# Kernel optimization log

Measured on AMD Instinct MI355X. Metric: run time of the kernel, lower is better.

Reference implementation:

```python
import jax, jax.numpy as jnp
import numpy as np

N_ROOMS = 300
N = N_ROOMS + 2          # state dim: 2 envelope nodes + rooms
M = N_ROOMS + 1          # input dim: [Tout; Q per room]
T = 60000                # number of t_eval points
DT = 30.0                # seconds between solution points
N_KNOTS = 2001           # Tout interpolation knots
ONE_THIRD = 1.0 / 3.0


def setup_inputs() -> dict:
    key = jax.random.key(0)
    k1, k2, k3, k4 = jax.random.split(key, 4)
    n_params = N * N + N_ROOMS
    params = jax.random.uniform(k1, (n_params,), jnp.float32)
    theta_lo = jnp.zeros((n_params,), jnp.float32)
    # conductance-like entries kept tiny so RK4 with h=30s stays stable
    theta_hi = jnp.concatenate([
        jnp.full((N * N,), 1e-4, jnp.float32),
        jnp.ones((N_ROOMS,), jnp.float32),
    ])
    B = jax.random.normal(k2, (N, M), jnp.float32) * 1e-3  # constant input matrix
    tout_t = jnp.linspace(0.0, T * DT, N_KNOTS).astype(jnp.float32)
    tout_vals = 15.0 + 10.0 * jax.random.normal(k3, (N_KNOTS,), jnp.float32)
    iv = 15.0 + 10.0 * jax.random.uniform(k4, (N, 1), jnp.float32)
    t_eval = jnp.arange(T, dtype=jnp.float32) * DT
    return {"params": params, "theta_lo": theta_lo, "theta_hi": theta_hi,
            "B": B, "tout_t": tout_t, "tout_vals": tout_vals,
            "iv": iv, "t_eval": t_eval, "t0": 0}


def reference(params, theta_lo, theta_hi, B, tout_t, tout_vals, iv, t_eval, t0):
    # transform + physical scaling of raw parameters
    x = jax.nn.sigmoid(params)
    theta = theta_lo + (theta_hi - theta_lo) * x
    W = theta[: N * N].reshape(N, N)
    # RC conductance matrix: diagonally dominant, negative diagonal (stable)
    A = W - jnp.diag(jnp.abs(W).sum(axis=1))
    Q = theta[N * N:]  # per-room heat gains [N_ROOMS]

    def f(t, y):
        # dy/dt = A y + B u,  u = [Tout(t + t0); Q]
        Tout = jnp.interp(t + t0, tout_t, tout_vals)
        u = jnp.concatenate([Tout[None], Q])[:, None]  # [M, 1]
        return A @ y + B @ u

    def step(y, th):
        # torchdiffeq method='rk4' uses the 3/8-rule (rk4_alt_step_func)
        t, h = th
        k1 = f(t, y)
        k2 = f(t + h * ONE_THIRD, y + h * ONE_THIRD * k1)
        k3 = f(t + 2.0 * h * ONE_THIRD, y + h * (k2 - ONE_THIRD * k1))
        k4 = f(t + h, y + h * (k1 - k2 + k3))
        y1 = y + (k1 + 3.0 * (k2 + k3) + k4) * (h * 0.125)
        return y1, y1

    ts = t_eval[:-1]
    hs = t_eval[1:] - t_eval[:-1]
    _, ys = jax.lax.scan(step, iv, (ts, hs))
    return jnp.concatenate([iv[None], ys], axis=0)  # [T, N, 1]
```

## Files before the change

kernel.cpp:

```cpp
#include <hip/hip_runtime.h>
#include <math.h>

#define NN     302
#define MM     301
#define NROOMS 300
#define NP     320
#define TS     59999
#define KN     2001
#define DTH    30.0f

#define L_CHUNK 256
#define N_CHUNK 235
#define N_BND   234
#define NB_PAD  240
#define N_GRP   15

#define WS_M    0
#define WS_M2   102400
#define WS_P    307200
#define WS_UV   409600
#define WS_B0C  411200
#define WS_TAU  412160
#define WS_W    652160
#define WS_G    1061760
#define WS_Y    1138560
#define WS_Z    1213760
#define WS_SA   1218880
#define WS_SB   1257280
#define WS_PL   1276480
#define WS_PA   1378880
#define WS_PB   1481280
#define WS_PT   1583680
#define WS_MT   2914880

typedef float vf2 __attribute__((ext_vector_type(2)));

#define ENGINE_BOUNDS __launch_bounds__(512) __attribute__((amdgpu_waves_per_eu(2, 2)))
#define PKFMA(acc, a, b) asm("v_pk_fma_f32 %0, %1, %2, %0" : "+v"(acc) : "v"(a), "v"(b))
#define PIN4(a, b, c, d) asm volatile("" : "+v"(a), "+v"(b), "+v"(c), "+v"(d))

__global__ __launch_bounds__(320) void buildrow_kernel(
    const float* __restrict__ params, const float* __restrict__ tlo,
    const float* __restrict__ thi, float* __restrict__ M, float* __restrict__ MT)
{
    const int r = blockIdx.x;
    const int c = threadIdx.x;
    float wv = 0.0f;
    if (r < NN && c < NN) {
        const int idx = r * NN + c;
        const float x = 1.0f / (1.0f + expf(-params[idx]));
        wv = tlo[idx] + (thi[idx] - tlo[idx]) * x;
    }
    __shared__ float red[5];
    float s = fabsf(wv);
    #pragma unroll
    for (int off = 32; off > 0; off >>= 1) s += __shfl_xor(s, off, 64);
    if ((c & 63) == 0) red[c >> 6] = s;
    __syncthreads();
    const float rs = red[0] + red[1] + red[2] + red[3] + red[4];
    float v = DTH * wv;
    if (r == c) v -= DTH * rs;
    M[r * NP + c] = v;
    MT[(size_t)c * NP + r] = v;
}

__global__ void b0c_kernel(const float* __restrict__ params,
                           const float* __restrict__ tlo,
                           const float* __restrict__ thi,
                           const float* __restrict__ B, float* __restrict__ b0c)
{
    __shared__ float Qs[NROOMS];
    const int r = blockIdx.x;
    const int l = threadIdx.x;
    for (int q = l; q < NROOMS; q += 64) {
        const int idx = NN * NN + q;
        const float x = 1.0f / (1.0f + expf(-params[idx]));
        Qs[q] = tlo[idx] + (thi[idx] - tlo[idx]) * x;
    }
    __syncthreads();
    if (r >= NN) {
        if (l == 0) { b0c[r] = 0.0f; b0c[NP + r] = 0.0f; }
        return;
    }
    float s = 0.0f;
    for (int q = l; q < NROOMS; q += 64) s = fmaf(B[r * MM + 1 + q], Qs[q], s);
    #pragma unroll
    for (int off = 32; off > 0; off >>= 1) s += __shfl_xor(s, off, 64);
    if (l == 0) { b0c[r] = B[r * MM]; b0c[NP + r] = s; }
}

__global__ void matmul4r(const float* __restrict__ A, const float* __restrict__ B,
                         float* __restrict__ C)
{
    const int c = blockIdx.x * 64 + threadIdx.x;
    const int r0 = blockIdx.y * 4;
    const float* Ar = A + (size_t)r0 * NP;
    float a0 = 0.f, a1 = 0.f, a2 = 0.f, a3 = 0.f;
    #pragma unroll 4
    for (int k = 0; k < NP; ++k) {
        const float b = B[(size_t)k * NP + c];
        a0 = fmaf(Ar[k], b, a0);
        a1 = fmaf(Ar[NP + k], b, a1);
        a2 = fmaf(Ar[2 * NP + k], b, a2);
        a3 = fmaf(Ar[3 * NP + k], b, a3);
    }
    C[(size_t)r0 * NP + c] = a0;
    C[(size_t)(r0 + 1) * NP + c] = a1;
    C[(size_t)(r0 + 2) * NP + c] = a2;
    C[(size_t)(r0 + 3) * NP + c] = a3;
}

__global__ void matmulP(const float* __restrict__ M2, const float* __restrict__ M,
                        float* __restrict__ P, float* __restrict__ PT0)
{
    const int c = blockIdx.x * 64 + threadIdx.x;
    const int r0 = blockIdx.y * 4;
    const float* Ar = M2 + (size_t)r0 * NP;
    float a0 = 0.f, a1 = 0.f, a2 = 0.f, a3 = 0.f;
    #pragma unroll 4
    for (int k = 0; k < NP; ++k) {
        const size_t o = (size_t)k * NP + c;
        const float b = (1.0f / 6.0f) * M[o] + (1.0f / 24.0f) * M2[o];
        a0 = fmaf(Ar[k], b, a0);
        a1 = fmaf(Ar[NP + k], b, a1);
        a2 = fmaf(Ar[2 * NP + k], b, a2);
        a3 = fmaf(Ar[3 * NP + k], b, a3);
    }
    float acc[4] = {a0, a1, a2, a3};
    float4 t;
    #pragma unroll
    for (int u = 0; u < 4; ++u) {
        const int r = r0 + u;
        const size_t idx = (size_t)r * NP + c;
        float v = acc[u] + M[idx] + 0.5f * M2[idx];
        if (r == c && r < NN) v += 1.0f;
        P[idx] = v;
        ((float*)&t)[u] = v;
    }
    *(float4*)(PT0 + (size_t)c * NP + r0) = t;
}

__global__ __launch_bounds__(320) void vec_kernel(
    const float* __restrict__ MT, const float* __restrict__ b0c,
    float* __restrict__ uv, const float* __restrict__ iv,
    float* __restrict__ W, float* __restrict__ out)
{
    __shared__ float ysB[NP], ysC[NP];
    const int tid = threadIdx.x;
    const float s = DTH / 8.0f;

    const float b0 = b0c[tid];
    const float cc = b0c[NP + tid];
    ysB[tid] = b0; ysC[tid] = cc;
    __syncthreads();

    float mb, mc, m2b, m2c, m3b, m3c;
    {
        float aB = 0.f, aC = 0.f;
        for (int k = 0; k < NP; ++k) {
            const float a = MT[(size_t)k * NP + tid];
            aB = fmaf(a, ysB[k], aB);
            aC = fmaf(a, ysC[k], aC);
        }
        mb = aB; mc = aC;
    }
    __syncthreads(); ysB[tid] = mb; ysC[tid] = mc; __syncthreads();
    {
        float aB = 0.f, aC = 0.f;
        for (int k = 0; k < NP; ++k) {
            const float a = MT[(size_t)k * NP + tid];
            aB = fmaf(a, ysB[k], aB);
            aC = fmaf(a, ysC[k], aC);
        }
        m2b = aB; m2c = aC;
    }
    __syncthreads(); ysB[tid] = m2b; ysC[tid] = m2c; __syncthreads();
    {
        float aB = 0.f, aC = 0.f;
        for (int k = 0; k < NP; ++k) {
            const float a = MT[(size_t)k * NP + tid];
            aB = fmaf(a, ysB[k], aB);
            aC = fmaf(a, ysC[k], aC);
        }
        m3b = aB; m3c = aC;
    }

    const float u1 = s * (b0 + mb + (1.0f / 3.0f) * (m2b + m3b));
    const float u2 = s * (3.0f * b0 + 2.0f * mb + m2b);
    const float u3 = s * (3.0f * b0 + mb);
    const float u4 = s * b0;
    const float dd = s * (8.0f * cc + 4.0f * mc + (4.0f / 3.0f) * m2c + (1.0f / 3.0f) * m3c);

    uv[tid]          = u1;
    uv[NP + tid]     = u2;
    uv[2 * NP + tid] = u3;
    uv[3 * NP + tid] = u4;
    uv[4 * NP + tid] = dd;

    W[(size_t)(0 << 8) * NP + tid] = dd;
    W[(size_t)(1 << 8) * NP + tid] = u1;
    W[(size_t)(2 << 8) * NP + tid] = u2;
    W[(size_t)(3 << 8) * NP + tid] = u3;
    W[(size_t)(4 << 8) * NP + tid] = u4;

    if (tid < NN) out[tid] = iv[tid];
}

__global__ void tau_kernel(const float* __restrict__ tout_t,
                           const float* __restrict__ tout_v,
                           const int* __restrict__ t0p,
                           float4* __restrict__ tau)
{
    const int n = blockIdx.x * 256 + threadIdx.x;
    if (n >= TS) return;
    const float tbase = 30.0f * (float)n + (float)(*t0p);
    float r[4];
    #pragma unroll
    for (int st = 0; st < 4; ++st) {
        const float x = tbase + 10.0f * (float)st;
        float res;
        if (x <= tout_t[0])            res = tout_v[0];
        else if (x >= tout_t[KN - 1])  res = tout_v[KN - 1];
        else {
            int k = (int)(x * (1.0f / 900.0f));
            if (k > KN - 2) k = KN - 2;
            if (k < 0) k = 0;
            if (x < tout_t[k] && k > 0) --k;
            else if (x >= tout_t[k + 1] && k < KN - 2) ++k;
            const float tk = tout_t[k], tk1 = tout_t[k + 1];
            const float wgt = (x - tk) / (tk1 - tk);
            res = tout_v[k] + wgt * (tout_v[k + 1] - tout_v[k]);
        }
        r[st] = res;
    }
    tau[n] = make_float4(r[0], r[1], r[2], r[3]);
}

__global__ __launch_bounds__(320) void fat_kernel(
    const float* __restrict__ src, float* __restrict__ dst,
    float* __restrict__ PTall, int j, float* __restrict__ W,
    const float* __restrict__ Sin, float* __restrict__ Sout, int npairs)
{
    const int b = blockIdx.x;
    const int tid = threadIdx.x;
    if (b < 320) {
        const int w = tid >> 6, l = tid & 63;
        const int r = (b & 63) * 5 + w;
        const int c = (b >> 6) * 64 + l;
        const float* Ar = src + (size_t)r * NP;
        float acc = 0.f;
        #pragma unroll 4
        for (int k = 0; k < NP; ++k)
            acc = fmaf(Ar[k], src[(size_t)k * NP + c], acc);
        dst[(size_t)r * NP + c] = acc;
        PTall[(size_t)(j + 1) * NP * NP + (size_t)c * NP + r] = acc;
        return;
    }
    const float* PTj = PTall + (size_t)j * NP * NP;
    const int c0 = (b - 320) * 4;
    __shared__ float ys[4][NP];
    if (j < 8) {
        const int nc = 5 << j;
        #pragma unroll
        for (int u = 0; u < 4; ++u) {
            const int ci = c0 + u;
            float val = 0.0f;
            if (ci < nc) {
                const int v = ci >> j, mo = ci & ((1 << j) - 1);
                val = W[(size_t)((v << 8) + mo) * NP + tid];
            }
            ys[u][tid] = val;
        }
        __syncthreads();
        float a0 = 0.f, a1 = 0.f, a2 = 0.f, a3 = 0.f;
        #pragma unroll 4
        for (int k = 0; k < NP; ++k) {
            const float p = PTj[(size_t)k * NP + tid];
            a0 = fmaf(p, ys[0][k], a0);
            a1 = fmaf(p, ys[1][k], a1);
            a2 = fmaf(p, ys[2][k], a2);
            a3 = fmaf(p, ys[3][k], a3);
        }
        const float acc[4] = {a0, a1, a2, a3};
        #pragma unroll
        for (int u = 0; u < 4; ++u) {
            const int ci = c0 + u;
            if (ci < nc) {
                const int v = ci >> j, mo = ci & ((1 << j) - 1);
                W[(size_t)((v << 8) + (1 << j) + mo) * NP + tid] = acc[u];
            }
        }
    } else {
        #pragma unroll
        for (int u = 0; u < 4; ++u) {
            const int k = c0 + u;
            ys[u][tid] = (k < npairs) ? Sin[(size_t)(2 * k) * NP + tid] : 0.0f;
        }
        __syncthreads();
        float a0 = 0.f, a1 = 0.f, a2 = 0.f, a3 = 0.f;
        #pragma unroll 4
        for (int k = 0; k < NP; ++k) {
            const float p = PTj[(size_t)k * NP + tid];
            a0 = fmaf(p, ys[0][k], a0);
            a1 = fmaf(p, ys[1][k], a1);
            a2 = fmaf(p, ys[2][k], a2);
            a3 = fmaf(p, ys[3][k], a3);
        }
        const float acc[4] = {a0, a1, a2, a3};
        #pragma unroll
        for (int u = 0; u < 4; ++u) {
            const int k = c0 + u;
            if (k < npairs)
                Sout[(size_t)k * NP + tid] = acc[u] + Sin[(size_t)(2 * k + 1) * NP + tid];
        }
    }
}

__global__ void gsum_kernel(const float* __restrict__ W,
                            const float4* __restrict__ tau,
                            float* __restrict__ G)
{
    const int r = blockIdx.x * 64 + threadIdx.x;
    const int c = blockIdx.y;
    if (c >= N_BND) { G[(size_t)c * NP + r] = 0.0f; return; }
    const float* W0 = W;
    const float* W1 = W + 1 * (size_t)L_CHUNK * NP;
    const float* W2 = W + 2 * (size_t)L_CHUNK * NP;
    const float* W3 = W + 3 * (size_t)L_CHUNK * NP;
    const float* W4 = W + 4 * (size_t)L_CHUNK * NP;
    const int nbase = c * L_CHUNK + L_CHUNK - 1;
    float g = 0.f;
    for (int m = 0; m < L_CHUNK; ++m) {
        const float4 a = tau[nbase - m];
        const size_t o = (size_t)m * NP + r;
        float t = W0[o];
        t = fmaf(a.x, W1[o], t);
        t = fmaf(a.y, W2[o], t);
        t = fmaf(a.z, W3[o], t);
        t = fmaf(a.w, W4[o], t);
        g += t;
    }
    G[(size_t)c * NP + r] = g;
}

__device__ __forceinline__ void load_pfrag(const float* __restrict__ Psrc,
                                           vf2 p[5][20], int l, int w)
{
    #pragma unroll
    for (int k = 0; k < 5; ++k) {
        const float* Pr = Psrc + (size_t)(l + 64 * k) * NP + 40 * w;
        #pragma unroll
        for (int j4 = 0; j4 < 10; ++j4) {
            const float4 v4 = *(const float4*)(Pr + 4 * j4);
            vf2 a; a.x = v4.x; a.y = v4.y;
            vf2 b; b.x = v4.z; b.y = v4.w;
            p[k][2 * j4] = a;
            p[k][2 * j4 + 1] = b;
        }
    }
    #pragma unroll
    for (int k = 0; k < 5; ++k)
        #pragma unroll
        for (int jj = 0; jj < 20; jj += 4)
            PIN4(p[k][jj], p[k][jj + 1], p[k][jj + 2], p[k][jj + 3]);
}

__device__ __forceinline__ float step_matvec(vf2 p[5][20],
                                             const float* __restrict__ ybuf,
                                             float* __restrict__ partial,
                                             int tid, int w, int l)
{
    vf2 a0 = {0.f, 0.f}, a1 = {0.f, 0.f}, a2 = {0.f, 0.f},
        a3 = {0.f, 0.f}, a4 = {0.f, 0.f};
    const float* yb = ybuf + 40 * w;
    #pragma unroll
    for (int j4 = 0; j4 < 10; ++j4) {
        const float4 yv = *(const float4*)(yb + 4 * j4);
        vf2 y01; y01.x = yv.x; y01.y = yv.y;
        vf2 y23; y23.x = yv.z; y23.y = yv.w;
        const int jj = 2 * j4;
        PKFMA(a0, p[0][jj], y01); PKFMA(a0, p[0][jj + 1], y23);
        PKFMA(a1, p[1][jj], y01); PKFMA(a1, p[1][jj + 1], y23);
        PKFMA(a2, p[2][jj], y01); PKFMA(a2, p[2][jj + 1], y23);
        PKFMA(a3, p[3][jj], y01); PKFMA(a3, p[3][jj + 1], y23);
        PKFMA(a4, p[4][jj], y01); PKFMA(a4, p[4][jj + 1], y23);
    }
    float* pw = partial + w * NP;
    pw[l]       = a0.x + a0.y;
    pw[l + 64]  = a1.x + a1.y;
    pw[l + 128] = a2.x + a2.y;
    pw[l + 192] = a3.x + a3.y;
    pw[l + 256] = a4.x + a4.y;
    __syncthreads();
    float s = 0.f;
    if (tid < NP) {
        #pragma unroll
        for (int k = 0; k < 8; ++k) s += partial[k * NP + tid];
    }
    return s;
}

__global__ ENGINE_BOUNDS void bscan_kernel(
    const float* __restrict__ PL16, const float* __restrict__ S4,
    const float* __restrict__ iv, float* __restrict__ Z)
{
    const int tid = threadIdx.x;
    const int w = tid >> 6, l = tid & 63;
    vf2 p[5][20];
    load_pfrag(PL16, p, l, w);

    __shared__ float ybuf[NP];
    __shared__ float partial[8 * NP];
    if (tid < NP) { const float y0 = (tid < NN) ? iv[tid] : 0.f; ybuf[tid] = y0; Z[tid] = y0; }
    __syncthreads();

    for (int g = 0; g < N_GRP; ++g) {
        const float s = step_matvec(p, ybuf, partial, tid, w, l);
        if (tid < NP) {
            const float yn = s + S4[(size_t)g * NP + tid];
            ybuf[tid] = yn;
            Z[(size_t)(g + 1) * NP + tid] = yn;
        }
        __syncthreads();
    }
}

__global__ ENGINE_BOUNDS void brefill_kernel(
    const float* __restrict__ PL, const float* __restrict__ G,
    const float* __restrict__ Z, float* __restrict__ Y)
{
    const int tid = threadIdx.x;
    const int w = tid >> 6, l = tid & 63;
    vf2 p[5][20];
    load_pfrag(PL, p, l, w);

    __shared__ float ybuf[NP];
    __shared__ float partial[8 * NP];
    const int g = blockIdx.x;
    if (tid < NP) {
        const float z = Z[(size_t)g * NP + tid];
        ybuf[tid] = z;
        if (g == 0) Y[tid] = z;
    }
    __syncthreads();

    for (int i = 0; i < 16; ++i) {
        const int idx = 16 * g + i;
        if (idx >= N_BND) break;
        const float s = step_matvec(p, ybuf, partial, tid, w, l);
        if (tid < NP) {
            const float yn = s + G[(size_t)idx * NP + tid];
            ybuf[tid] = yn;
            Y[(size_t)(idx + 1) * NP + tid] = yn;
        }
        __syncthreads();
    }
}

__global__ ENGINE_BOUNDS void refill_kernel(
    const float* __restrict__ P, const float* __restrict__ uv,
    const float4* __restrict__ tau, const float* __restrict__ Y,
    float* __restrict__ out)
{
    const int tid = threadIdx.x;
    const int w = tid >> 6, l = tid & 63;
    vf2 p[5][20];
    load_pfrag(P, p, l, w);

    float du0 = 0.f, du1 = 0.f, du2 = 0.f, du3 = 0.f, dd = 0.f;
    if (tid < NP) {
        du0 = uv[tid]; du1 = uv[NP + tid]; du2 = uv[2 * NP + tid];
        du3 = uv[3 * NP + tid]; dd = uv[4 * NP + tid];
    }

    __shared__ float ybuf[NP];
    __shared__ float partial[8 * NP];
    const int c = blockIdx.x;
    if (tid < NP) ybuf[tid] = Y[(size_t)c * NP + tid];
    __syncthreads();

    const int n0 = c * L_CHUNK;
    const int n1 = (n0 + L_CHUNK < TS) ? (n0 + L_CHUNK) : TS;
    for (int n = n0; n < n1; ++n) {
        const float s = step_matvec(p, ybuf, partial, tid, w, l);
        if (tid < NP) {
            const float4 a = tau[n];
            float yn = s + dd;
            yn = fmaf(a.x, du0, yn);
            yn = fmaf(a.y, du1, yn);
            yn = fmaf(a.z, du2, yn);
            yn = fmaf(a.w, du3, yn);
            ybuf[tid] = yn;
            if (tid < NN) out[(size_t)(n + 1) * NN + tid] = yn;
        }
        __syncthreads();
    }
}

extern "C" void kernel_launch(void* const* d_in, const int* in_sizes, int n_in,
                              void* d_out, int out_size, void* d_ws, size_t ws_size,
                              hipStream_t stream)
{
    const float* params = (const float*)d_in[0];
    const float* tlo    = (const float*)d_in[1];
    const float* thi    = (const float*)d_in[2];
    const float* B      = (const float*)d_in[3];
    const float* tout_t = (const float*)d_in[4];
    const float* tout_v = (const float*)d_in[5];
    const float* iv     = (const float*)d_in[6];
    const int*   t0     = (const int*)d_in[8];
    float* out = (float*)d_out;
    float* ws  = (float*)d_ws;

    float*  M    = ws + WS_M;
    float*  MT   = ws + WS_MT;
    float*  M2   = ws + WS_M2;
    float*  P    = ws + WS_P;
    float*  UV   = ws + WS_UV;
    float*  B0C  = ws + WS_B0C;
    float4* TAU  = (float4*)(ws + WS_TAU);
    float*  W    = ws + WS_W;
    float*  G    = ws + WS_G;
    float*  Y    = ws + WS_Y;
    float*  Z    = ws + WS_Z;
    float*  SA   = ws + WS_SA;
    float*  SB   = ws + WS_SB;
    float*  PL   = ws + WS_PL;
    float*  PA   = ws + WS_PA;
    float*  PB   = ws + WS_PB;
    float*  PT   = ws + WS_PT;

    buildrow_kernel<<<NP, NP, 0, stream>>>(params, tlo, thi, M, MT);
    b0c_kernel<<<NP, 64, 0, stream>>>(params, tlo, thi, B, B0C);

    matmul4r<<<dim3(5, 80), 64, 0, stream>>>(M, M, M2);
    matmulP<<<dim3(5, 80), 64, 0, stream>>>(M2, M, P, PT);

    vec_kernel<<<1, NP, 0, stream>>>(MT, B0C, UV, iv, W, out);
    tau_kernel<<<(TS + 255) / 256, 256, 0, stream>>>(tout_t, tout_v, t0, TAU);

    const float* Spp[5] = { G, SA, SB, SA, SB };
    const float* src = P;
    for (int j = 0; j < 8; ++j) {
        float* dst = (j == 7) ? PL : ((j & 1) ? PB : PA);
        const int aux = ((5 << j) + 3) / 4;
        fat_kernel<<<320 + aux, 320, 0, stream>>>(src, dst, PT, j, W,
                                                  nullptr, nullptr, 0);
        src = dst;
    }
    gsum_kernel<<<dim3(5, NB_PAD), 64, 0, stream>>>(W, TAU, G);
    for (int j = 8; j < 12; ++j) {
        float* dst = (j & 1) ? PB : PA;
        const int npairs = 120 >> (j - 8);
        const int aux = (npairs + 3) / 4;
        fat_kernel<<<320 + aux, 320, 0, stream>>>(src, dst, PT, j, W,
                                                  Spp[j - 8], (float*)Spp[j - 7], npairs);
        src = dst;
    }

    bscan_kernel<<<1, 512, 0, stream>>>(PB, SB, iv, Z);
    brefill_kernel<<<N_GRP, 512, 0, stream>>>(PL, G, Z, Y);

    refill_kernel<<<N_CHUNK, 512, 0, stream>>>(P, UV, TAU, Y, out);
}
```

Baseline: 827.6 us.

## Halve per-step barriers via wave-local reduction and batched ring-buffer stores

Each wave now reduces the 40 rows of the state vector it will itself read next step. Only one block barrier is needed per step, and the partial-sum buffer is double-buffered so the next step's writes cannot race the current step's reads. Output rows go into a shared-memory ring and are flushed every 16 steps. Per-step inputs (S4, G, tau) are prefetched into registers or shared memory. This cuts barrier and global-latency cost on the serial recurrence, at the price of more shared memory and periodic flush bursts.

```diff
diff --git a/kernel.cpp b/kernel.cpp
--- a/kernel.cpp
+++ b/kernel.cpp
@@ -365,14 +365,11 @@
             PIN4(p[k][jj], p[k][jj + 1], p[k][jj + 2], p[k][jj + 3]);
 }
 
-__device__ __forceinline__ float step_matvec(vf2 p[5][20],
-                                             const float* __restrict__ ybuf,
-                                             float* __restrict__ partial,
-                                             int tid, int w, int l)
+__device__ __forceinline__ void fma_phase(vf2 p[5][20], const float* __restrict__ yb,
+                                          float* __restrict__ pw, int l)
 {
     vf2 a0 = {0.f, 0.f}, a1 = {0.f, 0.f}, a2 = {0.f, 0.f},
         a3 = {0.f, 0.f}, a4 = {0.f, 0.f};
-    const float* yb = ybuf + 40 * w;
     #pragma unroll
     for (int j4 = 0; j4 < 10; ++j4) {
         const float4 yv = *(const float4*)(yb + 4 * j4);
@@ -385,18 +382,18 @@
         PKFMA(a3, p[3][jj], y01); PKFMA(a3, p[3][jj + 1], y23);
         PKFMA(a4, p[4][jj], y01); PKFMA(a4, p[4][jj + 1], y23);
     }
-    float* pw = partial + w * NP;
     pw[l]       = a0.x + a0.y;
     pw[l + 64]  = a1.x + a1.y;
     pw[l + 128] = a2.x + a2.y;
     pw[l + 192] = a3.x + a3.y;
     pw[l + 256] = a4.x + a4.y;
-    __syncthreads();
-    float s = 0.f;
-    if (tid < NP) {
-        #pragma unroll
-        for (int k = 0; k < 8; ++k) s += partial[k * NP + tid];
-    }
+}
+
+__device__ __forceinline__ float reduce8(const float* __restrict__ pb, int r)
+{
+    float s = pb[r];
+    #pragma unroll
+    for (int k = 1; k < 8; ++k) s += pb[k * NP + r];
     return s;
 }
 
@@ -410,19 +407,36 @@
     load_pfrag(PL16, p, l, w);
 
     __shared__ float ybuf[NP];
-    __shared__ float partial[8 * NP];
-    if (tid < NP) { const float y0 = (tid < NN) ? iv[tid] : 0.f; ybuf[tid] = y0; Z[tid] = y0; }
+    __shared__ float part[2 * 8 * NP];
+    __shared__ float ring[N_GRP * NP];
+
+    const int r = 40 * w + l;
+    float Sv[N_GRP];
+    if (l < 40) {
+        #pragma unroll
+        for (int i = 0; i < N_GRP; ++i) Sv[i] = S4[(size_t)i * NP + r];
+    }
+    if (tid < NP) {
+        const float y0 = (tid < NN) ? iv[tid] : 0.f;
+        ybuf[tid] = y0;
+        Z[tid] = y0;
+    }
     __syncthreads();
 
     for (int g = 0; g < N_GRP; ++g) {
-        const float s = step_matvec(p, ybuf, partial, tid, w, l);
-        if (tid < NP) {
-            const float yn = s + S4[(size_t)g * NP + tid];
-            ybuf[tid] = yn;
-            Z[(size_t)(g + 1) * NP + tid] = yn;
-        }
+        float* pb = part + (g & 1) * 8 * NP;
+        fma_phase(p, ybuf + 40 * w, pb + w * NP, l);
         __syncthreads();
-    }
+        if (l < 40) {
+            const float yn = reduce8(pb, r) + Sv[g];
+            ybuf[r] = yn;
+            ring[g * NP + r] = yn;
+        }
+    }
+    __syncthreads();
+    for (int s2 = 0; s2 < N_GRP; ++s2)
+        for (int j = tid; j < NP; j += 512)
+            Z[(size_t)(s2 + 1) * NP + j] = ring[s2 * NP + j];
 }
 
 __global__ ENGINE_BOUNDS void brefill_kernel(
@@ -435,8 +449,16 @@
     load_pfrag(PL, p, l, w);
 
     __shared__ float ybuf[NP];
-    __shared__ float partial[8 * NP];
+    __shared__ float part[2 * 8 * NP];
+    __shared__ float ring[16 * NP];
+
     const int g = blockIdx.x;
+    const int nsteps = (16 * g + 16 <= N_BND) ? 16 : (N_BND - 16 * g);
+    const int r = 40 * w + l;
+    float Gv[16];
+    if (l < 40) {
+        for (int i = 0; i < nsteps; ++i) Gv[i] = G[(size_t)(16 * g + i) * NP + r];
+    }
     if (tid < NP) {
         const float z = Z[(size_t)g * NP + tid];
         ybuf[tid] = z;
@@ -444,17 +466,20 @@
     }
     __syncthreads();
 
-    for (int i = 0; i < 16; ++i) {
-        const int idx = 16 * g + i;
-        if (idx >= N_BND) break;
-        const float s = step_matvec(p, ybuf, partial, tid, w, l);
-        if (tid < NP) {
-            const float yn = s + G[(size_t)idx * NP + tid];
-            ybuf[tid] = yn;
-            Y[(size_t)(idx + 1) * NP + tid] = yn;
-        }
+    for (int i = 0; i < nsteps; ++i) {
+        float* pb = part + (i & 1) * 8 * NP;
+        fma_phase(p, ybuf + 40 * w, pb + w * NP, l);
         __syncthreads();
-    }
+        if (l < 40) {
+            const float yn = reduce8(pb, r) + Gv[i];
+            ybuf[r] = yn;
+            ring[i * NP + r] = yn;
+        }
+    }
+    __syncthreads();
+    for (int s2 = 0; s2 < nsteps; ++s2)
+        for (int j = tid; j < NP; j += 512)
+            Y[(size_t)(16 * g + 1 + s2) * NP + j] = ring[s2 * NP + j];
 }
 
 __global__ ENGINE_BOUNDS void refill_kernel(
@@ -467,33 +492,52 @@
     vf2 p[5][20];
     load_pfrag(P, p, l, w);
 
+    __shared__ float ybuf[NP];
+    __shared__ float part[2 * 8 * NP];
+    __shared__ float ring[16 * NP];
+    __shared__ float4 taus[16];
+
+    const int r = 40 * w + l;
     float du0 = 0.f, du1 = 0.f, du2 = 0.f, du3 = 0.f, dd = 0.f;
-    if (tid < NP) {
-        du0 = uv[tid]; du1 = uv[NP + tid]; du2 = uv[2 * NP + tid];
-        du3 = uv[3 * NP + tid]; dd = uv[4 * NP + tid];
-    }
-
-    __shared__ float ybuf[NP];
-    __shared__ float partial[8 * NP];
+    if (l < 40) {
+        du0 = uv[r]; du1 = uv[NP + r]; du2 = uv[2 * NP + r];
+        du3 = uv[3 * NP + r]; dd = uv[4 * NP + r];
+    }
+
     const int c = blockIdx.x;
-    if (tid < NP) ybuf[tid] = Y[(size_t)c * NP + tid];
-    __syncthreads();
-
     const int n0 = c * L_CHUNK;
     const int n1 = (n0 + L_CHUNK < TS) ? (n0 + L_CHUNK) : TS;
+    if (tid < NP) ybuf[tid] = Y[(size_t)c * NP + tid];
+    int wstart = n0;
+    if (tid < 16 && n0 + tid < n1) taus[tid] = tau[n0 + tid];
+    __syncthreads();
+
     for (int n = n0; n < n1; ++n) {
-        const float s = step_matvec(p, ybuf, partial, tid, w, l);
-        if (tid < NP) {
-            const float4 a = tau[n];
-            float yn = s + dd;
+        const int slot = n - wstart;
+        float* pb = part + (n & 1) * 8 * NP;
+        fma_phase(p, ybuf + 40 * w, pb + w * NP, l);
+        __syncthreads();
+        if (l < 40) {
+            const float4 a = taus[slot];
+            float yn = reduce8(pb, r) + dd;
             yn = fmaf(a.x, du0, yn);
             yn = fmaf(a.y, du1, yn);
             yn = fmaf(a.z, du2, yn);
             yn = fmaf(a.w, du3, yn);
-            ybuf[tid] = yn;
-            if (tid < NN) out[(size_t)(n + 1) * NN + tid] = yn;
-        }
-        __syncthreads();
+            ybuf[r] = yn;
+            ring[slot * NP + r] = yn;
+        }
+        if (slot == 15 || n == n1 - 1) {
+            __syncthreads();
+            const int nrows = slot + 1;
+            for (int s2 = 0; s2 < nrows; ++s2) {
+                const size_t row = (size_t)(wstart + 1 + s2);
+                for (int j = tid; j < NN; j += 512)
+                    out[row * NN + j] = ring[s2 * NP + j];
+            }
+            wstart = n + 1;
+            if (tid < 16 && wstart + tid < n1) taus[tid] = tau[wstart + tid];
+        }
     }
 }
 
```

Measured after the change: 820.0 us. Within noise of the previous version (-0.9%).
